# Performance work log

Hardware: AMD Instinct MI355X
Metric: run time of the kernel (lower is better)

Reference implementation:

```python
import jax, jax.numpy as jnp
import numpy as np

V = 50000      # variables -> 2V literals
C = 200000     # clauses
E = 300000     # edges per polarity
EMB = 128
NFC = 3
ROUNDS = 26


def setup_inputs() -> dict:
    key = jax.random.key(0)
    ks = jax.random.split(key, 16)
    s = 0.05
    f32 = jnp.float32
    inp = {
        "l_pos_emb": jax.random.normal(ks[0], (V, EMB), f32) * s,
        "l_neg_emb": jax.random.normal(ks[1], (V, EMB), f32) * s,
        "c_emb": jax.random.normal(ks[2], (C, EMB), f32) * s,
        "l_mlp_W": jax.random.normal(ks[3], (NFC, EMB, EMB), f32) * s,
        "l_mlp_b": jnp.zeros((NFC, EMB), f32),
        "c_mlp_W": jax.random.normal(ks[4], (NFC, EMB, EMB), f32) * s,
        "c_mlp_b": jnp.zeros((NFC, EMB), f32),
        "l_Wih": jax.random.normal(ks[5], (4 * EMB, 2 * EMB), f32) * s,
        "l_Whh": jax.random.normal(ks[6], (4 * EMB, EMB), f32) * s,
        "l_bih": jnp.zeros((4 * EMB,), f32),
        "l_bhh": jnp.zeros((4 * EMB,), f32),
        "c_Wih": jax.random.normal(ks[7], (4 * EMB, EMB), f32) * s,
        "c_Whh": jax.random.normal(ks[8], (4 * EMB, EMB), f32) * s,
        "c_bih": jnp.zeros((4 * EMB,), f32),
        "c_bhh": jnp.zeros((4 * EMB,), f32),
        "pos_src": jax.random.randint(ks[9], (E,), 0, V, jnp.int32),
        "pos_dst": jax.random.randint(ks[10], (E,), 0, C, jnp.int32),
        "neg_src": jax.random.randint(ks[11], (E,), 0, V, jnp.int32),
        "neg_dst": jax.random.randint(ks[12], (E,), 0, C, jnp.int32),
    }
    return inp


def _mlp(x, W, b):
    # num_fc Linear layers with ReLU between (no final activation)
    n = W.shape[0]
    for i in range(n):
        x = x @ W[i] + b[i]
        if i < n - 1:
            x = jax.nn.relu(x)
    return x


def _lstm_cell(x, h, c, Wih, Whh, bih, bhh):
    # torch nn.LSTM single step; gate order i, f, g, o
    gates = x @ Wih.T + h @ Whh.T + bih + bhh
    i, f, g, o = jnp.split(gates, 4, axis=1)
    c_new = jax.nn.sigmoid(f) * c + jax.nn.sigmoid(i) * jnp.tanh(g)
    h_new = jax.nn.sigmoid(o) * jnp.tanh(c_new)
    return h_new, c_new


def reference(l_pos_emb, l_neg_emb, c_emb,
              l_mlp_W, l_mlp_b, c_mlp_W, c_mlp_b,
              l_Wih, l_Whh, l_bih, l_bhh,
              c_Wih, c_Whh, c_bih, c_bhh,
              pos_src, pos_dst, neg_src, neg_dst):
    num_v = l_pos_emb.shape[0]
    num_c = c_emb.shape[0]
    l_h = jnp.concatenate([l_pos_emb, l_neg_emb], axis=0)   # [2V, E]
    l_c = jnp.zeros_like(l_h)
    c_h = c_emb
    c_c = jnp.zeros_like(c_h)

    def round_fn(carry, _):
        l_h, l_c, c_h, c_c = carry
        # literal -> clause messages
        l_msg = _mlp(l_h, l_mlp_W, l_mlp_b)
        pos_msg, neg_msg = l_msg[:num_v], l_msg[num_v:]
        l2c = (jax.ops.segment_sum(pos_msg[pos_src], pos_dst, num_segments=num_c)
               + jax.ops.segment_sum(neg_msg[neg_src], neg_dst, num_segments=num_c))
        # clause -> literal messages (reverse edges)
        c_msg = _mlp(c_h, c_mlp_W, c_mlp_b)
        pos_c2l = jax.ops.segment_sum(c_msg[pos_dst], pos_src, num_segments=num_v)
        neg_c2l = jax.ops.segment_sum(c_msg[neg_dst], neg_src, num_segments=num_v)
        c2l = jnp.concatenate([pos_c2l, neg_c2l], axis=0)    # [2V, E]
        # flip literal hidden (pair each literal with its negation)
        flip = jnp.concatenate([l_h[num_v:], l_h[:num_v]], axis=0)
        l_x = jnp.concatenate([c2l, flip], axis=1)           # [2V, 2E]
        l_h, l_c = _lstm_cell(l_x, l_h, l_c, l_Wih, l_Whh, l_bih, l_bhh)
        c_h, c_c = _lstm_cell(l2c, c_h, c_c, c_Wih, c_Whh, c_bih, c_bhh)
        return (l_h, l_c, c_h, c_c), None

    (l_h, l_c, c_h, c_c), _ = jax.lax.scan(round_fn, (l_h, l_c, c_h, c_c),
                                           None, length=ROUNDS)
    # concat final literal and clause embeddings: [2V + C, EMB]
    return jnp.concatenate([l_h, c_h], axis=0)
```

## Files before the change

### kernel.cpp

```cpp
#include <hip/hip_runtime.h>
#include <math.h>

typedef __attribute__((ext_vector_type(8))) short short8;
typedef __attribute__((ext_vector_type(4))) float f32x4;

constexpr int NV = 50000;
constexpr int NL = 100000;
constexpr int NC = 200000;
constexpr int NE = 300000;
constexpr int NROUNDS = 26;

__device__ __forceinline__ float sigf(float x) { return 1.0f / (1.0f + __expf(-x)); }

__device__ __forceinline__ void split8(const float* a, short8& h, short8& l) {
#pragma unroll
    for (int j = 0; j < 8; j++) {
        unsigned u = __float_as_uint(a[j]);
        h[j] = (short)(u >> 16);
        float lf = a[j] - __uint_as_float(u & 0xffff0000u);
        l[j] = (short)(__float_as_uint(lf) >> 16);
    }
}
__device__ __forceinline__ void split1(float x, unsigned short* h, unsigned short* l) {
    unsigned u = __float_as_uint(x);
    *h = (unsigned short)(u >> 16);
    float lf = x - __uint_as_float(u & 0xffff0000u);
    *l = (unsigned short)(__float_as_uint(lf) >> 16);
}

__device__ __forceinline__ void splitw(float x, unsigned short* h, unsigned short* l) {
    unsigned u = __float_as_uint(x);
    unsigned hr = (u + 0x7fffu + ((u >> 16) & 1u)) & 0xffff0000u;
    float lf = x - __uint_as_float(hr);
    unsigned ul = __float_as_uint(lf);
    *h = (unsigned short)(hr >> 16);
    *l = (unsigned short)((ul + 0x7fffu + ((ul >> 16) & 1u)) >> 16);
}


__global__ __launch_bounds__(256) void pack_mlp_frag(
    const float* __restrict__ W, unsigned short* __restrict__ Wh, unsigned short* __restrict__ Wl)
{
    int fid = blockIdx.x * 256 + threadIdx.x;
    if (fid >= 6144) return;
    int lane = fid & 63;
    int tile = (fid >> 6) & 7;
    int kt = (fid >> 9) & 3;
    int layer = fid >> 11;
    int l15 = lane & 15, lg = lane >> 4;
    int n = tile * 16 + l15;
#pragma unroll
    for (int j = 0; j < 8; j++) {
        int k = kt * 32 + lg * 8 + j;
        unsigned short h, l;
        splitw(W[layer * 16384 + k * 128 + n], &h, &l);
        Wh[(size_t)fid * 8 + j] = h;
        Wl[(size_t)fid * 8 + j] = l;
    }
}

__global__ __launch_bounds__(256) void pack_lstm_frag(
    const float* __restrict__ Wih, const float* __restrict__ Whh, int kih, int nstep,
    unsigned short* __restrict__ Wh, unsigned short* __restrict__ Wl)
{
    int fid = blockIdx.x * 256 + threadIdx.x;
    if (fid >= nstep * 2048) return;
    int lane = fid & 63;
    int tile = (fid >> 6) & 31;
    int kt = fid >> 11;
    int l15 = lane & 15, lg = lane >> 4;
    int n = tile * 16 + l15;
#pragma unroll
    for (int j = 0; j < 8; j++) {
        int k = kt * 32 + lg * 8 + j;
        float v = (k < kih) ? Wih[n * kih + k] : Whh[(n << 7) + (k - kih)];
        unsigned short h, l;
        splitw(v, &h, &l);
        Wh[(size_t)fid * 8 + j] = h;
        Wl[(size_t)fid * 8 + j] = l;
    }
}

__global__ __launch_bounds__(256) void csr_hist_k(
    const int* __restrict__ ps, const int* __restrict__ pd,
    const int* __restrict__ ns, const int* __restrict__ nd,
    int* __restrict__ cnt_c, int* __restrict__ cnt_l)
{
    int e = blockIdx.x * 256 + threadIdx.x;
    if (e >= NE) return;
    atomicAdd(&cnt_c[pd[e]], 1);
    atomicAdd(&cnt_c[nd[e]], 1);
    atomicAdd(&cnt_l[ps[e]], 1);
    atomicAdd(&cnt_l[NV + ns[e]], 1);
}

__global__ __launch_bounds__(256) void scan_p1(
    const int* __restrict__ cnt, int* __restrict__ partials, int n)
{
    __shared__ int sdata[256];
    int t = threadIdx.x, b = blockIdx.x;
    int base = b * 1024 + t * 4;
    int s = 0;
#pragma unroll
    for (int j = 0; j < 4; j++) { int i = base + j; if (i < n) s += cnt[i]; }
    sdata[t] = s; __syncthreads();
    for (int st = 128; st > 0; st >>= 1) {
        if (t < st) sdata[t] += sdata[t + st];
        __syncthreads();
    }
    if (t == 0) partials[b] = sdata[0];
}

__global__ __launch_bounds__(256) void scan_p2(int* __restrict__ partials, int nb, int* __restrict__ rowptr_end)
{
    __shared__ int sdata[256];
    int t = threadIdx.x;
    int v = (t < nb) ? partials[t] : 0;
    int x = v;
    sdata[t] = x; __syncthreads();
    for (int st = 1; st < 256; st <<= 1) {
        int y = (t >= st) ? sdata[t - st] : 0;
        __syncthreads();
        x += y; sdata[t] = x;
        __syncthreads();
    }
    if (t < nb) partials[t] = x - v;
    if (t == 255) *rowptr_end = sdata[255];
}

__global__ __launch_bounds__(256) void scan_p3(
    const int* __restrict__ cnt, const int* __restrict__ partials,
    int* __restrict__ rowptr, int* __restrict__ cursor, int n)
{
    __shared__ int sdata[256];
    int t = threadIdx.x, b = blockIdx.x;
    int base = b * 1024 + t * 4;
    int v[4]; int s = 0;
#pragma unroll
    for (int j = 0; j < 4; j++) { int i = base + j; v[j] = (i < n) ? cnt[i] : 0; s += v[j]; }
    int x = s;
    sdata[t] = x; __syncthreads();
    for (int st = 1; st < 256; st <<= 1) {
        int y = (t >= st) ? sdata[t - st] : 0;
        __syncthreads();
        x += y; sdata[t] = x;
        __syncthreads();
    }
    int off = partials[b] + x - s;
#pragma unroll
    for (int j = 0; j < 4; j++) {
        int i = base + j;
        if (i < n) { rowptr[i] = off; cursor[i] = off; off += v[j]; }
    }
}

__global__ __launch_bounds__(256) void csr_fill_k(
    const int* __restrict__ ps, const int* __restrict__ pd,
    const int* __restrict__ ns, const int* __restrict__ nd,
    int* __restrict__ cur_c, int* __restrict__ eidx_c,
    int* __restrict__ cur_l, int* __restrict__ eidx_l)
{
    int e = blockIdx.x * 256 + threadIdx.x;
    if (e >= NE) return;
    int p;
    p = atomicAdd(&cur_c[pd[e]], 1); eidx_c[p] = ps[e];
    p = atomicAdd(&cur_c[nd[e]], 1); eidx_c[p] = NV + ns[e];
    p = atomicAdd(&cur_l[ps[e]], 1); eidx_l[p] = pd[e];
    p = atomicAdd(&cur_l[NV + ns[e]], 1); eidx_l[p] = nd[e];
}

__global__ __launch_bounds__(256) void gather_sum_k(
    const float* __restrict__ msg, const int* __restrict__ rowptr,
    const int* __restrict__ eidx, float* __restrict__ out, int nrows)
{
    int row = (blockIdx.x * 256 + threadIdx.x) >> 6;
    if (row >= nrows) return;
    int lane = threadIdx.x & 63;
    int beg = rowptr[row], end = rowptr[row + 1];
    float ax = 0.f, ay = 0.f;
    for (int j = beg; j < end; j++) {
        int src = eidx[j];
        float2 v = *reinterpret_cast<const float2*>(msg + (size_t)src * 128 + lane * 2);
        ax += v.x; ay += v.y;
    }
    *reinterpret_cast<float2*>(out + (size_t)row * 128 + lane * 2) = make_float2(ax, ay);
}

__global__ __launch_bounds__(256, 3) void mlp3_v4(
    const float* __restrict__ x, const unsigned short* __restrict__ Wh,
    const unsigned short* __restrict__ Wl, const float* __restrict__ bias,
    float* __restrict__ y, int M)
{
    __shared__ unsigned short Xh[64][136];
    __shared__ unsigned short Xl[64][136];
    const int t = threadIdx.x;
    const int rb = blockIdx.x * 64;
    const int lane = t & 63, w = t >> 6, wr = w >> 1, wc = w & 1;
    const int l15 = lane & 15, lg = lane >> 4;

#pragma unroll
    for (int j = 0; j < 8; j++) {
        int i = t + 256 * j;
        int r = i >> 5, c4 = i & 31;
        int gr = rb + r; if (gr >= M) gr = M - 1;
        float4 v = *reinterpret_cast<const float4*>(x + (size_t)gr * 128 + c4 * 4);
        const float* vp = &v.x;
#pragma unroll
        for (int e = 0; e < 4; e++) {
            unsigned short h, l;
            split1(vp[e], &h, &l);
            Xh[r][c4 * 4 + e] = h;
            Xl[r][c4 * 4 + e] = l;
        }
    }
    __syncthreads();

    for (int layer = 0; layer < 3; layer++) {
        f32x4 acc[2][4];
#pragma unroll
        for (int m = 0; m < 2; m++)
#pragma unroll
            for (int nf = 0; nf < 4; nf++) acc[m][nf] = f32x4{0.f, 0.f, 0.f, 0.f};

        short8 bh[4], bl[4], bhn[4], bln[4];
#pragma unroll
        for (int nf = 0; nf < 4; nf++) {
            int tile = wc * 4 + nf;
            size_t off = ((size_t)((layer * 4 + 0) * 8 + tile) * 64 + lane) * 8;
            bh[nf] = *reinterpret_cast<const short8*>(Wh + off);
            bl[nf] = *reinterpret_cast<const short8*>(Wl + off);
        }

#pragma unroll
        for (int kt = 0; kt < 4; kt++) {
            short8 ah[2], al[2];
#pragma unroll
            for (int m = 0; m < 2; m++) {
                int row = wr * 32 + m * 16 + l15;
                ah[m] = *reinterpret_cast<const short8*>(&Xh[row][kt * 32 + lg * 8]);
                al[m] = *reinterpret_cast<const short8*>(&Xl[row][kt * 32 + lg * 8]);
            }
            if (kt < 3) {
#pragma unroll
                for (int nf = 0; nf < 4; nf++) {
                    int tile = wc * 4 + nf;
                    size_t off = ((size_t)((layer * 4 + kt + 1) * 8 + tile) * 64 + lane) * 8;
                    bhn[nf] = *reinterpret_cast<const short8*>(Wh + off);
                    bln[nf] = *reinterpret_cast<const short8*>(Wl + off);
                }
            }
#pragma unroll
            for (int nf = 0; nf < 4; nf++)
#pragma unroll
                for (int m = 0; m < 2; m++)
                    acc[m][nf] = __builtin_amdgcn_mfma_f32_16x16x32_bf16(ah[m], bh[nf], acc[m][nf], 0, 0, 0);
#pragma unroll
            for (int nf = 0; nf < 4; nf++)
#pragma unroll
                for (int m = 0; m < 2; m++)
                    acc[m][nf] = __builtin_amdgcn_mfma_f32_16x16x32_bf16(ah[m], bl[nf], acc[m][nf], 0, 0, 0);
#pragma unroll
            for (int nf = 0; nf < 4; nf++)
#pragma unroll
                for (int m = 0; m < 2; m++)
                    acc[m][nf] = __builtin_amdgcn_mfma_f32_16x16x32_bf16(al[m], bh[nf], acc[m][nf], 0, 0, 0);
            if (kt < 3) {
#pragma unroll
                for (int nf = 0; nf < 4; nf++) { bh[nf] = bhn[nf]; bl[nf] = bln[nf]; }
            }
        }

        float bv[4];
#pragma unroll
        for (int nf = 0; nf < 4; nf++) bv[nf] = bias[layer * 128 + wc * 64 + nf * 16 + l15];
        __syncthreads();
        if (layer < 2) {
#pragma unroll
            for (int m = 0; m < 2; m++)
#pragma unroll
                for (int nf = 0; nf < 4; nf++)
#pragma unroll
                    for (int rr = 0; rr < 4; rr++) {
                        float v = fmaxf(acc[m][nf][rr] + bv[nf], 0.f);
                        unsigned short h, l;
                        split1(v, &h, &l);
                        int rw = wr * 32 + m * 16 + lg * 4 + rr;
                        int cl = wc * 64 + nf * 16 + l15;
                        Xh[rw][cl] = h;
                        Xl[rw][cl] = l;
                    }
            __syncthreads();
        } else {
#pragma unroll
            for (int m = 0; m < 2; m++)
#pragma unroll
                for (int rr = 0; rr < 4; rr++) {
                    int gr = rb + wr * 32 + m * 16 + lg * 4 + rr;
                    if (gr < M) {
#pragma unroll
                        for (int nf = 0; nf < 4; nf++)
                            y[(size_t)gr * 128 + wc * 64 + nf * 16 + l15] = acc[m][nf][rr] + bv[nf];
                    }
                }
        }
    }
}

template <int NKT, bool FLIP>
__global__ __launch_bounds__(256, 2) void lstm_v5(
    const float* __restrict__ A0, const float* __restrict__ A1, const float* __restrict__ A2,
    const unsigned short* __restrict__ Bh_g, const unsigned short* __restrict__ Bl_g,
    const float* __restrict__ bih, const float* __restrict__ bhh,
    float* __restrict__ c_st, float* __restrict__ h_out, int M)
{
    __shared__ float As[2][4096];
    __shared__ unsigned short Bsm[2][8192];
    const int t = threadIdx.x;
    const int s = blockIdx.x;
    const int rb = blockIdx.y * 128;
    const int lane = t & 63, w = t >> 6, wr = w >> 1, wc = w & 1;
    const int l15 = lane & 15, lg = lane >> 4;

    f32x4 acc[4][4];
#pragma unroll
    for (int m = 0; m < 4; m++)
#pragma unroll
        for (int g = 0; g < 4; g++) acc[m][g] = f32x4{0.f, 0.f, 0.f, 0.f};

#pragma unroll
    for (int i = 0; i < 4; i++) {
        int idx = t + 256 * i;
        int r = idx >> 3, c4 = idx & 7;
        int gr = rb + r; if (gr >= M) gr = M - 1;
        float4 v = *reinterpret_cast<const float4*>(A0 + (size_t)gr * 128 + c4 * 4);
        int off = (r * 128 + c4 * 16) ^ ((r & 7) << 4);
        *reinterpret_cast<float4*>((char*)As[0] + off) = v;
    }
#pragma unroll
    for (int i = 0; i < 4; i++) {
        int idx = t + 256 * i;
        int f = idx >> 6, ln = idx & 63;
        int sel = f >> 3, ft = f & 7;
        int gt = (ft >> 1) * 8 + s * 2 + (ft & 1);
        const unsigned short* bsrc = sel ? Bl_g : Bh_g;
        uint4 v = *reinterpret_cast<const uint4*>(bsrc + ((size_t)gt * 64 + ln) * 8);
        *reinterpret_cast<uint4*>((char*)Bsm[0] + idx * 16) = v;
    }
    __syncthreads();

    int cur = 0;
#pragma unroll
    for (int kt = 0; kt < NKT; kt++) {
        float4 a_stg[4]; uint4 b_stg[4];
        if (kt + 1 < NKT) {
            const int kn = kt + 1;
            const int seg = kn >> 2;
            const float* src = (seg == 0) ? A0 : ((seg == 1) ? A1 : A2);
            const bool useF = FLIP && (seg == 1);
            const int kco = (kn & 3) * 32;
#pragma unroll
            for (int i = 0; i < 4; i++) {
                int idx = t + 256 * i;
                int r = idx >> 3, c4 = idx & 7;
                int gr = rb + r; if (gr >= M) gr = M - 1;
                if (useF) gr = (gr < NV) ? gr + NV : gr - NV;
                a_stg[i] = *reinterpret_cast<const float4*>(src + (size_t)gr * 128 + kco + c4 * 4);
            }
#pragma unroll
            for (int i = 0; i < 4; i++) {
                int idx = t + 256 * i;
                int f = idx >> 6, ln = idx & 63;
                int sel = f >> 3, ft = f & 7;
                int gt = (ft >> 1) * 8 + s * 2 + (ft & 1);
                const unsigned short* bsrc = sel ? Bl_g : Bh_g;
                b_stg[i] = *reinterpret_cast<const uint4*>(bsrc + ((size_t)(kn * 32 + gt) * 64 + ln) * 8);
            }
        }

        const char* Ab = (const char*)As[cur];
        short8 ah[4], al[4];
#pragma unroll
        for (int m = 0; m < 4; m++) {
            int r = wr * 64 + m * 16 + l15;
            int base = r * 128 + lg * 32;
            int swz = (r & 7) << 4;
            float av[8];
            *reinterpret_cast<float4*>(&av[0]) =
                *reinterpret_cast<const float4*>(Ab + (base ^ swz));
            *reinterpret_cast<float4*>(&av[4]) =
                *reinterpret_cast<const float4*>(Ab + ((base + 16) ^ swz));
            split8(av, ah[m], al[m]);
        }
        const char* Bb = (const char*)Bsm[cur];
#pragma unroll
        for (int g = 0; g < 4; g++) {
            short8 bh = *reinterpret_cast<const short8*>(Bb + ((g * 2 + wc) * 64 + lane) * 16);
            short8 bl = *reinterpret_cast<const short8*>(Bb + ((8 + g * 2 + wc) * 64 + lane) * 16);
#pragma unroll
            for (int m = 0; m < 4; m++)
                acc[m][g] = __builtin_amdgcn_mfma_f32_16x16x32_bf16(ah[m], bh, acc[m][g], 0, 0, 0);
#pragma unroll
            for (int m = 0; m < 4; m++)
                acc[m][g] = __builtin_amdgcn_mfma_f32_16x16x32_bf16(ah[m], bl, acc[m][g], 0, 0, 0);
#pragma unroll
            for (int m = 0; m < 4; m++)
                acc[m][g] = __builtin_amdgcn_mfma_f32_16x16x32_bf16(al[m], bh, acc[m][g], 0, 0, 0);
        }

        if (kt + 1 < NKT) {
            int nb = cur ^ 1;
#pragma unroll
            for (int i = 0; i < 4; i++) {
                int idx = t + 256 * i;
                int r = idx >> 3, c4 = idx & 7;
                int off = (r * 128 + c4 * 16) ^ ((r & 7) << 4);
                *reinterpret_cast<float4*>((char*)As[nb] + off) = a_stg[i];
            }
#pragma unroll
            for (int i = 0; i < 4; i++) {
                int idx = t + 256 * i;
                *reinterpret_cast<uint4*>((char*)Bsm[nb] + idx * 16) = b_stg[i];
            }
        }
        __syncthreads();
        cur ^= 1;
    }

    const int colc = s * 32 + wc * 16 + l15;
    float bs4[4];
#pragma unroll
    for (int g = 0; g < 4; g++) bs4[g] = bih[g * 128 + colc] + bhh[g * 128 + colc];
#pragma unroll
    for (int m = 0; m < 4; m++)
#pragma unroll
        for (int rr = 0; rr < 4; rr++) {
            int gr = rb + wr * 64 + m * 16 + lg * 4 + rr;
            if (gr >= M) continue;
            float gi = acc[m][0][rr] + bs4[0];
            float gf = acc[m][1][rr] + bs4[1];
            float gg = acc[m][2][rr] + bs4[2];
            float go = acc[m][3][rr] + bs4[3];
            size_t p = (size_t)gr * 128 + colc;
            float cold = c_st[p];
            float cn = sigf(gf) * cold + sigf(gi) * tanhf(gg);
            float hn = sigf(go) * tanhf(cn);
            c_st[p] = cn;
            h_out[p] = hn;
        }
}

extern "C" void kernel_launch(void* const* d_in, const int* in_sizes, int n_in,
                              void* d_out, int out_size, void* d_ws, size_t ws_size,
                              hipStream_t stream)
{
    const float* l_pos   = (const float*)d_in[0];
    const float* l_neg   = (const float*)d_in[1];
    const float* c_emb   = (const float*)d_in[2];
    const float* l_mlp_W = (const float*)d_in[3];
    const float* l_mlp_b = (const float*)d_in[4];
    const float* c_mlp_W = (const float*)d_in[5];
    const float* c_mlp_b = (const float*)d_in[6];
    const float* l_Wih   = (const float*)d_in[7];
    const float* l_Whh   = (const float*)d_in[8];
    const float* l_bih   = (const float*)d_in[9];
    const float* l_bhh   = (const float*)d_in[10];
    const float* c_Wih   = (const float*)d_in[11];
    const float* c_Whh   = (const float*)d_in[12];
    const float* c_bih   = (const float*)d_in[13];
    const float* c_bhh   = (const float*)d_in[14];
    const int* pos_src   = (const int*)d_in[15];
    const int* pos_dst   = (const int*)d_in[16];
    const int* neg_src   = (const int*)d_in[17];
    const int* neg_dst   = (const int*)d_in[18];

    float* out  = (float*)d_out;
    float* l_hA = out;
    float* c_hP = out + (size_t)NL * 128;

    float* wsp = (float*)d_ws;
    float* l_hB  = wsp; wsp += (size_t)NL * 128;
    float* l_c   = wsp; wsp += (size_t)NL * 128;
    float* c_c   = wsp; wsp += (size_t)NC * 128;
    float* l_msg = wsp; wsp += (size_t)NL * 128;
    float* c_hQ  = wsp; wsp += (size_t)NC * 128;
    float* l2c   = wsp; wsp += (size_t)NC * 128;
    float* c2l = l_msg;

    unsigned short* us = (unsigned short*)wsp;
    unsigned short* mlpLh = us; us += 3 * 128 * 128;
    unsigned short* mlpLl = us; us += 3 * 128 * 128;
    unsigned short* mlpCh = us; us += 3 * 128 * 128;
    unsigned short* mlpCl = us; us += 3 * 128 * 128;
    unsigned short* lstmLh = us; us += 512 * 384;
    unsigned short* lstmLl = us; us += 512 * 384;
    unsigned short* lstmCh = us; us += 512 * 256;
    unsigned short* lstmCl = us; us += 512 * 256;

    int* ip = (int*)us;
    int* cnt_c    = ip; ip += NC;
    int* rowptr_c = ip; ip += NC + 1;
    int* cur_c    = ip; ip += NC;
    int* eidx_c   = ip; ip += 2 * NE;
    int* cnt_l    = ip; ip += NL;
    int* rowptr_l = ip; ip += NL + 1;
    int* cur_l    = ip; ip += NL;
    int* eidx_l   = ip; ip += 2 * NE;
    int* part_c   = ip; ip += 256;
    int* part_l   = ip; ip += 256;

    hipMemcpyAsync(l_hA, l_pos, (size_t)NV * 128 * 4, hipMemcpyDeviceToDevice, stream);
    hipMemcpyAsync(l_hA + (size_t)NV * 128, l_neg, (size_t)NV * 128 * 4, hipMemcpyDeviceToDevice, stream);
    hipMemcpyAsync(c_hP, c_emb, (size_t)NC * 128 * 4, hipMemcpyDeviceToDevice, stream);
    hipMemsetAsync(l_c, 0, (size_t)NL * 128 * 4, stream);
    hipMemsetAsync(c_c, 0, (size_t)NC * 128 * 4, stream);

    pack_mlp_frag<<<24, 256, 0, stream>>>(l_mlp_W, mlpLh, mlpLl);
    pack_mlp_frag<<<24, 256, 0, stream>>>(c_mlp_W, mlpCh, mlpCl);
    pack_lstm_frag<<<96, 256, 0, stream>>>(l_Wih, l_Whh, 256, 12, lstmLh, lstmLl);
    pack_lstm_frag<<<64, 256, 0, stream>>>(c_Wih, c_Whh, 128, 8, lstmCh, lstmCl);

    hipMemsetAsync(cnt_c, 0, NC * sizeof(int), stream);
    hipMemsetAsync(cnt_l, 0, NL * sizeof(int), stream);
    constexpr int EB = (NE + 255) / 256;
    csr_hist_k<<<EB, 256, 0, stream>>>(pos_src, pos_dst, neg_src, neg_dst, cnt_c, cnt_l);
    constexpr int NBC = (NC + 1023) / 1024;
    constexpr int NBL = (NL + 1023) / 1024;
    scan_p1<<<NBC, 256, 0, stream>>>(cnt_c, part_c, NC);
    scan_p2<<<1, 256, 0, stream>>>(part_c, NBC, rowptr_c + NC);
    scan_p3<<<NBC, 256, 0, stream>>>(cnt_c, part_c, rowptr_c, cur_c, NC);
    scan_p1<<<NBL, 256, 0, stream>>>(cnt_l, part_l, NL);
    scan_p2<<<1, 256, 0, stream>>>(part_l, NBL, rowptr_l + NL);
    scan_p3<<<NBL, 256, 0, stream>>>(cnt_l, part_l, rowptr_l, cur_l, NL);
    csr_fill_k<<<EB, 256, 0, stream>>>(pos_src, pos_dst, neg_src, neg_dst,
                                       cur_c, eidx_c, cur_l, eidx_l);

    float* l_cur = l_hA;
    float* l_nxt = l_hB;
    float* c_cur = c_hP;
    float* c_oth = c_hQ;

    for (int r = 0; r < NROUNDS; r++) {
        mlp3_v4<<<(NL + 63) / 64, 256, 0, stream>>>(l_cur, mlpLh, mlpLl, l_mlp_b, l_msg, NL);
        mlp3_v4<<<(NC + 63) / 64, 256, 0, stream>>>(c_cur, mlpCh, mlpCl, c_mlp_b, c_oth, NC);

        gather_sum_k<<<NC * 64 / 256, 256, 0, stream>>>(l_msg, rowptr_c, eidx_c, l2c, NC);
        gather_sum_k<<<NL * 64 / 256, 256, 0, stream>>>(c_oth, rowptr_l, eidx_l, c2l, NL);

        lstm_v5<12, true><<<dim3(4, (NL + 127) / 128), 256, 0, stream>>>(
            c2l, l_cur, l_cur, lstmLh, lstmLl, l_bih, l_bhh, l_c, l_nxt, NL);
        lstm_v5<8, false><<<dim3(4, (NC + 127) / 128), 256, 0, stream>>>(
            l2c, c_cur, nullptr, lstmCh, lstmCl, c_bih, c_bhh, c_c, c_oth, NC);

        float* t2 = l_cur; l_cur = l_nxt; l_nxt = t2;
        t2 = c_cur; c_cur = c_oth; c_oth = t2;
    }
    (void)in_sizes; (void)n_in; (void)out_size; (void)ws_size;
}
```

Measured before the change: 22.52 ms.

## Store activations as pre-split bf16 hi/lo planes instead of fp32

Hidden states, messages and aggregated sums now live in a split bf16 hi/lo layout (two 128-wide planes per row) rather than fp32. The MLP and LSTM kernels can then copy operands straight into shared memory in MFMA fragment order, with no per-tile split work. The LSTM A tile also drops its swizzled fp32 staging for a fragment-ordered layout. Gather sums reconstruct fp32 from the planes and re-split on output, and extra conversion kernels run at start and end. The lo plane is truncated rather than rounded, so some precision is lost compared with the fp32 path.

```diff
diff --git a/kernel.cpp b/kernel.cpp
--- a/kernel.cpp
+++ b/kernel.cpp
@@ -3,6 +3,7 @@
 
 typedef __attribute__((ext_vector_type(8))) short short8;
 typedef __attribute__((ext_vector_type(4))) float f32x4;
+typedef unsigned short ushort_t;
 
 constexpr int NV = 50000;
 constexpr int NL = 100000;
@@ -12,34 +13,50 @@
 
 __device__ __forceinline__ float sigf(float x) { return 1.0f / (1.0f + __expf(-x)); }
 
-__device__ __forceinline__ void split8(const float* a, short8& h, short8& l) {
-#pragma unroll
-    for (int j = 0; j < 8; j++) {
-        unsigned u = __float_as_uint(a[j]);
-        h[j] = (short)(u >> 16);
-        float lf = a[j] - __uint_as_float(u & 0xffff0000u);
-        l[j] = (short)(__float_as_uint(lf) >> 16);
-    }
-}
-__device__ __forceinline__ void split1(float x, unsigned short* h, unsigned short* l) {
+__device__ __forceinline__ void split1(float x, ushort_t* h, ushort_t* l) {
     unsigned u = __float_as_uint(x);
-    *h = (unsigned short)(u >> 16);
+    *h = (ushort_t)(u >> 16);
     float lf = x - __uint_as_float(u & 0xffff0000u);
-    *l = (unsigned short)(__float_as_uint(lf) >> 16);
-}
-
-__device__ __forceinline__ void splitw(float x, unsigned short* h, unsigned short* l) {
+    *l = (ushort_t)(__float_as_uint(lf) >> 16);
+}
+__device__ __forceinline__ float recf(ushort_t h, ushort_t l) {
+    return __uint_as_float((unsigned)h << 16) + __uint_as_float((unsigned)l << 16);
+}
+
+__device__ __forceinline__ void splitw(float x, ushort_t* h, ushort_t* l) {
     unsigned u = __float_as_uint(x);
     unsigned hr = (u + 0x7fffu + ((u >> 16) & 1u)) & 0xffff0000u;
     float lf = x - __uint_as_float(hr);
     unsigned ul = __float_as_uint(lf);
-    *h = (unsigned short)(hr >> 16);
-    *l = (unsigned short)((ul + 0x7fffu + ((ul >> 16) & 1u)) >> 16);
+    *h = (ushort_t)(hr >> 16);
+    *l = (ushort_t)((ul + 0x7fffu + ((ul >> 16) & 1u)) >> 16);
+}
+
+
+__global__ __launch_bounds__(256) void split_rows_k(
+    const float* __restrict__ src, ushort_t* __restrict__ dst, int total)
+{
+    for (int i = blockIdx.x * 256 + threadIdx.x; i < total; i += gridDim.x * 256) {
+        int row = i >> 7, c = i & 127;
+        ushort_t h, l;
+        split1(src[i], &h, &l);
+        dst[(size_t)row * 256 + c] = h;
+        dst[(size_t)row * 256 + 128 + c] = l;
+    }
+}
+
+__global__ __launch_bounds__(256) void convert_out_k(
+    const ushort_t* __restrict__ src, float* __restrict__ dst, int total)
+{
+    for (int i = blockIdx.x * 256 + threadIdx.x; i < total; i += gridDim.x * 256) {
+        int row = i >> 7, c = i & 127;
+        dst[i] = recf(src[(size_t)row * 256 + c], src[(size_t)row * 256 + 128 + c]);
+    }
 }
 
 
 __global__ __launch_bounds__(256) void pack_mlp_frag(
-    const float* __restrict__ W, unsigned short* __restrict__ Wh, unsigned short* __restrict__ Wl)
+    const float* __restrict__ W, ushort_t* __restrict__ Wh, ushort_t* __restrict__ Wl)
 {
     int fid = blockIdx.x * 256 + threadIdx.x;
     if (fid >= 6144) return;
@@ -52,7 +69,7 @@
 #pragma unroll
     for (int j = 0; j < 8; j++) {
         int k = kt * 32 + lg * 8 + j;
-        unsigned short h, l;
+        ushort_t h, l;
         splitw(W[layer * 16384 + k * 128 + n], &h, &l);
         Wh[(size_t)fid * 8 + j] = h;
         Wl[(size_t)fid * 8 + j] = l;
@@ -61,7 +78,7 @@
 
 __global__ __launch_bounds__(256) void pack_lstm_frag(
     const float* __restrict__ Wih, const float* __restrict__ Whh, int kih, int nstep,
-    unsigned short* __restrict__ Wh, unsigned short* __restrict__ Wl)
+    ushort_t* __restrict__ Wh, ushort_t* __restrict__ Wl)
 {
     int fid = blockIdx.x * 256 + threadIdx.x;
     if (fid >= nstep * 2048) return;
@@ -74,7 +91,7 @@
     for (int j = 0; j < 8; j++) {
         int k = kt * 32 + lg * 8 + j;
         float v = (k < kih) ? Wih[n * kih + k] : Whh[(n << 7) + (k - kih)];
-        unsigned short h, l;
+        ushort_t h, l;
         splitw(v, &h, &l);
         Wh[(size_t)fid * 8 + j] = h;
         Wl[(size_t)fid * 8 + j] = l;
@@ -170,29 +187,37 @@
 }
 
 __global__ __launch_bounds__(256) void gather_sum_k(
-    const float* __restrict__ msg, const int* __restrict__ rowptr,
-    const int* __restrict__ eidx, float* __restrict__ out, int nrows)
+    const ushort_t* __restrict__ msg, const int* __restrict__ rowptr,
+    const int* __restrict__ eidx, ushort_t* __restrict__ out, int nrows)
 {
     int row = (blockIdx.x * 256 + threadIdx.x) >> 6;
     if (row >= nrows) return;
     int lane = threadIdx.x & 63;
     int beg = rowptr[row], end = rowptr[row + 1];
-    float ax = 0.f, ay = 0.f;
+    float a0 = 0.f, a1 = 0.f;
     for (int j = beg; j < end; j++) {
         int src = eidx[j];
-        float2 v = *reinterpret_cast<const float2*>(msg + (size_t)src * 128 + lane * 2);
-        ax += v.x; ay += v.y;
-    }
-    *reinterpret_cast<float2*>(out + (size_t)row * 128 + lane * 2) = make_float2(ax, ay);
-}
-
-__global__ __launch_bounds__(256, 3) void mlp3_v4(
-    const float* __restrict__ x, const unsigned short* __restrict__ Wh,
-    const unsigned short* __restrict__ Wl, const float* __restrict__ bias,
-    float* __restrict__ y, int M)
-{
-    __shared__ unsigned short Xh[64][136];
-    __shared__ unsigned short Xl[64][136];
+        const ushort_t* p = msg + (size_t)src * 256 + lane * 2;
+        unsigned hp = *reinterpret_cast<const unsigned*>(p);
+        unsigned lp = *reinterpret_cast<const unsigned*>(p + 128);
+        a0 += __uint_as_float(hp << 16) + __uint_as_float(lp << 16);
+        a1 += __uint_as_float(hp & 0xffff0000u) + __uint_as_float(lp & 0xffff0000u);
+    }
+    ushort_t h0, l0, h1, l1;
+    split1(a0, &h0, &l0);
+    split1(a1, &h1, &l1);
+    ushort_t* op = out + (size_t)row * 256 + lane * 2;
+    *reinterpret_cast<unsigned*>(op) = (unsigned)h0 | ((unsigned)h1 << 16);
+    *reinterpret_cast<unsigned*>(op + 128) = (unsigned)l0 | ((unsigned)l1 << 16);
+}
+
+__global__ __launch_bounds__(256, 3) void mlp3_v5(
+    const ushort_t* __restrict__ x, const ushort_t* __restrict__ Wh,
+    const ushort_t* __restrict__ Wl, const float* __restrict__ bias,
+    ushort_t* __restrict__ y, int M)
+{
+    __shared__ ushort_t Xh[64][136];
+    __shared__ ushort_t Xl[64][136];
     const int t = threadIdx.x;
     const int rb = blockIdx.x * 64;
     const int lane = t & 63, w = t >> 6, wr = w >> 1, wc = w & 1;
@@ -200,18 +225,13 @@
 
 #pragma unroll
     for (int j = 0; j < 8; j++) {
-        int i = t + 256 * j;
-        int r = i >> 5, c4 = i & 31;
+        int idx = t + 256 * j;
+        int plane = idx >> 10, rem = idx & 1023;
+        int r = rem >> 4, c8 = (rem & 15) * 8;
         int gr = rb + r; if (gr >= M) gr = M - 1;
-        float4 v = *reinterpret_cast<const float4*>(x + (size_t)gr * 128 + c4 * 4);
-        const float* vp = &v.x;
-#pragma unroll
-        for (int e = 0; e < 4; e++) {
-            unsigned short h, l;
-            split1(vp[e], &h, &l);
-            Xh[r][c4 * 4 + e] = h;
-            Xl[r][c4 * 4 + e] = l;
-        }
+        uint4 v = *reinterpret_cast<const uint4*>(x + (size_t)gr * 256 + plane * 128 + c8);
+        ushort_t* dst = plane ? &Xl[r][c8] : &Xh[r][c8];
+        *reinterpret_cast<uint4*>(dst) = v;
     }
     __syncthreads();
 
@@ -282,7 +302,7 @@
 #pragma unroll
                     for (int rr = 0; rr < 4; rr++) {
                         float v = fmaxf(acc[m][nf][rr] + bv[nf], 0.f);
-                        unsigned short h, l;
+                        ushort_t h, l;
                         split1(v, &h, &l);
                         int rw = wr * 32 + m * 16 + lg * 4 + rr;
                         int cl = wc * 64 + nf * 16 + l15;
@@ -298,8 +318,14 @@
                     int gr = rb + wr * 32 + m * 16 + lg * 4 + rr;
                     if (gr < M) {
 #pragma unroll
-                        for (int nf = 0; nf < 4; nf++)
-                            y[(size_t)gr * 128 + wc * 64 + nf * 16 + l15] = acc[m][nf][rr] + bv[nf];
+                        for (int nf = 0; nf < 4; nf++) {
+                            float v = acc[m][nf][rr] + bv[nf];
+                            ushort_t h, l;
+                            split1(v, &h, &l);
+                            size_t p = (size_t)gr * 256 + wc * 64 + nf * 16 + l15;
+                            y[p] = h;
+                            y[p + 128] = l;
+                        }
                     }
                 }
         }
@@ -307,14 +333,14 @@
 }
 
 template <int NKT, bool FLIP>
-__global__ __launch_bounds__(256, 2) void lstm_v5(
-    const float* __restrict__ A0, const float* __restrict__ A1, const float* __restrict__ A2,
-    const unsigned short* __restrict__ Bh_g, const unsigned short* __restrict__ Bl_g,
+__global__ __launch_bounds__(256, 2) void lstm_v6(
+    const ushort_t* __restrict__ A0, const ushort_t* __restrict__ A1, const ushort_t* __restrict__ A2,
+    const ushort_t* __restrict__ Bh_g, const ushort_t* __restrict__ Bl_g,
     const float* __restrict__ bih, const float* __restrict__ bhh,
-    float* __restrict__ c_st, float* __restrict__ h_out, int M)
-{
-    __shared__ float As[2][4096];
-    __shared__ unsigned short Bsm[2][8192];
+    float* __restrict__ c_st, ushort_t* __restrict__ h_out, int M)
+{
+    __shared__ uint4 As[2][1024];
+    __shared__ uint4 Bs[2][1024];
     const int t = threadIdx.x;
     const int s = blockIdx.x;
     const int rb = blockIdx.y * 128;
@@ -330,11 +356,11 @@
 #pragma unroll
     for (int i = 0; i < 4; i++) {
         int idx = t + 256 * i;
-        int r = idx >> 3, c4 = idx & 7;
-        int gr = rb + r; if (gr >= M) gr = M - 1;
-        float4 v = *reinterpret_cast<const float4*>(A0 + (size_t)gr * 128 + c4 * 4);
-        int off = (r * 128 + c4 * 16) ^ ((r & 7) << 4);
-        *reinterpret_cast<float4*>((char*)As[0] + off) = v;
+        int plane = idx >> 9, rem = idx & 511;
+        int tile = rem >> 6, ln = rem & 63;
+        int gr = rb + tile * 16 + (ln & 15); if (gr >= M) gr = M - 1;
+        As[0][idx] = *reinterpret_cast<const uint4*>(
+            A0 + (size_t)gr * 256 + plane * 128 + (ln >> 4) * 8);
     }
 #pragma unroll
     for (int i = 0; i < 4; i++) {
@@ -342,29 +368,30 @@
         int f = idx >> 6, ln = idx & 63;
         int sel = f >> 3, ft = f & 7;
         int gt = (ft >> 1) * 8 + s * 2 + (ft & 1);
-        const unsigned short* bsrc = sel ? Bl_g : Bh_g;
-        uint4 v = *reinterpret_cast<const uint4*>(bsrc + ((size_t)gt * 64 + ln) * 8);
-        *reinterpret_cast<uint4*>((char*)Bsm[0] + idx * 16) = v;
+        const ushort_t* bsrc = sel ? Bl_g : Bh_g;
+        Bs[0][idx] = *reinterpret_cast<const uint4*>(bsrc + ((size_t)gt * 64 + ln) * 8);
     }
     __syncthreads();
 
     int cur = 0;
 #pragma unroll
     for (int kt = 0; kt < NKT; kt++) {
-        float4 a_stg[4]; uint4 b_stg[4];
+        uint4 a_stg[4], b_stg[4];
         if (kt + 1 < NKT) {
             const int kn = kt + 1;
             const int seg = kn >> 2;
-            const float* src = (seg == 0) ? A0 : ((seg == 1) ? A1 : A2);
+            const ushort_t* src = (seg == 0) ? A0 : ((seg == 1) ? A1 : A2);
             const bool useF = FLIP && (seg == 1);
             const int kco = (kn & 3) * 32;
 #pragma unroll
             for (int i = 0; i < 4; i++) {
                 int idx = t + 256 * i;
-                int r = idx >> 3, c4 = idx & 7;
-                int gr = rb + r; if (gr >= M) gr = M - 1;
+                int plane = idx >> 9, rem = idx & 511;
+                int tile = rem >> 6, ln = rem & 63;
+                int gr = rb + tile * 16 + (ln & 15); if (gr >= M) gr = M - 1;
                 if (useF) gr = (gr < NV) ? gr + NV : gr - NV;
-                a_stg[i] = *reinterpret_cast<const float4*>(src + (size_t)gr * 128 + kco + c4 * 4);
+                a_stg[i] = *reinterpret_cast<const uint4*>(
+                    src + (size_t)gr * 256 + plane * 128 + kco + (ln >> 4) * 8);
             }
 #pragma unroll
             for (int i = 0; i < 4; i++) {
@@ -372,30 +399,24 @@
                 int f = idx >> 6, ln = idx & 63;
                 int sel = f >> 3, ft = f & 7;
                 int gt = (ft >> 1) * 8 + s * 2 + (ft & 1);
-                const unsigned short* bsrc = sel ? Bl_g : Bh_g;
+                const ushort_t* bsrc = sel ? Bl_g : Bh_g;
                 b_stg[i] = *reinterpret_cast<const uint4*>(bsrc + ((size_t)(kn * 32 + gt) * 64 + ln) * 8);
             }
         }
 
-        const char* Ab = (const char*)As[cur];
+        const uint4* Ab = As[cur];
+        const uint4* Bb = Bs[cur];
         short8 ah[4], al[4];
 #pragma unroll
         for (int m = 0; m < 4; m++) {
-            int r = wr * 64 + m * 16 + l15;
-            int base = r * 128 + lg * 32;
-            int swz = (r & 7) << 4;
-            float av[8];
-            *reinterpret_cast<float4*>(&av[0]) =
-                *reinterpret_cast<const float4*>(Ab + (base ^ swz));
-            *reinterpret_cast<float4*>(&av[4]) =
-                *reinterpret_cast<const float4*>(Ab + ((base + 16) ^ swz));
-            split8(av, ah[m], al[m]);
-        }
-        const char* Bb = (const char*)Bsm[cur];
+            int tile = wr * 4 + m;
+            ah[m] = *reinterpret_cast<const short8*>(&Ab[tile * 64 + lane]);
+            al[m] = *reinterpret_cast<const short8*>(&Ab[512 + tile * 64 + lane]);
+        }
 #pragma unroll
         for (int g = 0; g < 4; g++) {
-            short8 bh = *reinterpret_cast<const short8*>(Bb + ((g * 2 + wc) * 64 + lane) * 16);
-            short8 bl = *reinterpret_cast<const short8*>(Bb + ((8 + g * 2 + wc) * 64 + lane) * 16);
+            short8 bh = *reinterpret_cast<const short8*>(&Bb[(g * 2 + wc) * 64 + lane]);
+            short8 bl = *reinterpret_cast<const short8*>(&Bb[(8 + g * 2 + wc) * 64 + lane]);
 #pragma unroll
             for (int m = 0; m < 4; m++)
                 acc[m][g] = __builtin_amdgcn_mfma_f32_16x16x32_bf16(ah[m], bh, acc[m][g], 0, 0, 0);
@@ -410,17 +431,9 @@
         if (kt + 1 < NKT) {
             int nb = cur ^ 1;
 #pragma unroll
-            for (int i = 0; i < 4; i++) {
-                int idx = t + 256 * i;
-                int r = idx >> 3, c4 = idx & 7;
-                int off = (r * 128 + c4 * 16) ^ ((r & 7) << 4);
-                *reinterpret_cast<float4*>((char*)As[nb] + off) = a_stg[i];
-            }
-#pragma unroll
-            for (int i = 0; i < 4; i++) {
-                int idx = t + 256 * i;
-                *reinterpret_cast<uint4*>((char*)Bsm[nb] + idx * 16) = b_stg[i];
-            }
+            for (int i = 0; i < 4; i++) As[nb][t + 256 * i] = a_stg[i];
+#pragma unroll
+            for (int i = 0; i < 4; i++) Bs[nb][t + 256 * i] = b_stg[i];
         }
         __syncthreads();
         cur ^= 1;
@@ -440,12 +453,16 @@
             float gf = acc[m][1][rr] + bs4[1];
             float gg = acc[m][2][rr] + bs4[2];
             float go = acc[m][3][rr] + bs4[3];
-            size_t p = (size_t)gr * 128 + colc;
-            float cold = c_st[p];
+            size_t pc = (size_t)gr * 128 + colc;
+            float cold = c_st[pc];
             float cn = sigf(gf) * cold + sigf(gi) * tanhf(gg);
             float hn = sigf(go) * tanhf(cn);
-            c_st[p] = cn;
-            h_out[p] = hn;
+            c_st[pc] = cn;
+            ushort_t hh, hl;
+            split1(hn, &hh, &hl);
+            size_t ph = (size_t)gr * 256 + colc;
+            h_out[ph] = hh;
+            h_out[ph + 128] = hl;
         }
 }
 
@@ -473,28 +490,28 @@
     const int* neg_src   = (const int*)d_in[17];
     const int* neg_dst   = (const int*)d_in[18];
 
-    float* out  = (float*)d_out;
-    float* l_hA = out;
-    float* c_hP = out + (size_t)NL * 128;
+    float* out = (float*)d_out;
+    ushort_t* l_hQ = (ushort_t*)d_out;
+    ushort_t* c_hQ = (ushort_t*)(out + (size_t)NL * 128);
 
     float* wsp = (float*)d_ws;
-    float* l_hB  = wsp; wsp += (size_t)NL * 128;
-    float* l_c   = wsp; wsp += (size_t)NL * 128;
-    float* c_c   = wsp; wsp += (size_t)NC * 128;
-    float* l_msg = wsp; wsp += (size_t)NL * 128;
-    float* c_hQ  = wsp; wsp += (size_t)NC * 128;
-    float* l2c   = wsp; wsp += (size_t)NC * 128;
-    float* c2l = l_msg;
-
-    unsigned short* us = (unsigned short*)wsp;
-    unsigned short* mlpLh = us; us += 3 * 128 * 128;
-    unsigned short* mlpLl = us; us += 3 * 128 * 128;
-    unsigned short* mlpCh = us; us += 3 * 128 * 128;
-    unsigned short* mlpCl = us; us += 3 * 128 * 128;
-    unsigned short* lstmLh = us; us += 512 * 384;
-    unsigned short* lstmLl = us; us += 512 * 384;
-    unsigned short* lstmCh = us; us += 512 * 256;
-    unsigned short* lstmCl = us; us += 512 * 256;
+    ushort_t* l_hP  = (ushort_t*)wsp; wsp += (size_t)NL * 128;
+    float*    l_c   = wsp;            wsp += (size_t)NL * 128;
+    float*    c_c   = wsp;            wsp += (size_t)NC * 128;
+    ushort_t* l_msg = (ushort_t*)wsp; wsp += (size_t)NL * 128;
+    ushort_t* c_hP  = (ushort_t*)wsp; wsp += (size_t)NC * 128;
+    ushort_t* l2c   = (ushort_t*)wsp; wsp += (size_t)NC * 128;
+    ushort_t* c2l = l_msg;
+
+    ushort_t* us = (ushort_t*)wsp;
+    ushort_t* mlpLh = us; us += 3 * 128 * 128;
+    ushort_t* mlpLl = us; us += 3 * 128 * 128;
+    ushort_t* mlpCh = us; us += 3 * 128 * 128;
+    ushort_t* mlpCl = us; us += 3 * 128 * 128;
+    ushort_t* lstmLh = us; us += 512 * 384;
+    ushort_t* lstmLl = us; us += 512 * 384;
+    ushort_t* lstmCh = us; us += 512 * 256;
+    ushort_t* lstmCl = us; us += 512 * 256;
 
     int* ip = (int*)us;
     int* cnt_c    = ip; ip += NC;
@@ -508,9 +525,9 @@
     int* part_c   = ip; ip += 256;
     int* part_l   = ip; ip += 256;
 
-    hipMemcpyAsync(l_hA, l_pos, (size_t)NV * 128 * 4, hipMemcpyDeviceToDevice, stream);
-    hipMemcpyAsync(l_hA + (size_t)NV * 128, l_neg, (size_t)NV * 128 * 4, hipMemcpyDeviceToDevice, stream);
-    hipMemcpyAsync(c_hP, c_emb, (size_t)NC * 128 * 4, hipMemcpyDeviceToDevice, stream);
+    split_rows_k<<<2048, 256, 0, stream>>>(l_pos, l_hP, NV * 128);
+    split_rows_k<<<2048, 256, 0, stream>>>(l_neg, l_hP + (size_t)NV * 256, NV * 128);
+    split_rows_k<<<2048, 256, 0, stream>>>(c_emb, c_hP, NC * 128);
     hipMemsetAsync(l_c, 0, (size_t)NL * 128 * 4, stream);
     hipMemsetAsync(c_c, 0, (size_t)NC * 128 * 4, stream);
 
@@ -534,25 +551,27 @@
     csr_fill_k<<<EB, 256, 0, stream>>>(pos_src, pos_dst, neg_src, neg_dst,
                                        cur_c, eidx_c, cur_l, eidx_l);
 
-    float* l_cur = l_hA;
-    float* l_nxt = l_hB;
-    float* c_cur = c_hP;
-    float* c_oth = c_hQ;
+    ushort_t* l_cur = l_hP;
+    ushort_t* l_nxt = l_hQ;
+    ushort_t* c_cur = c_hP;
+    ushort_t* c_oth = c_hQ;
 
     for (int r = 0; r < NROUNDS; r++) {
-        mlp3_v4<<<(NL + 63) / 64, 256, 0, stream>>>(l_cur, mlpLh, mlpLl, l_mlp_b, l_msg, NL);
-        mlp3_v4<<<(NC + 63) / 64, 256, 0, stream>>>(c_cur, mlpCh, mlpCl, c_mlp_b, c_oth, NC);
+        mlp3_v5<<<(NL + 63) / 64, 256, 0, stream>>>(l_cur, mlpLh, mlpLl, l_mlp_b, l_msg, NL);
+        mlp3_v5<<<(NC + 63) / 64, 256, 0, stream>>>(c_cur, mlpCh, mlpCl, c_mlp_b, c_oth, NC);
 
         gather_sum_k<<<NC * 64 / 256, 256, 0, stream>>>(l_msg, rowptr_c, eidx_c, l2c, NC);
         gather_sum_k<<<NL * 64 / 256, 256, 0, stream>>>(c_oth, rowptr_l, eidx_l, c2l, NL);
 
-        lstm_v5<12, true><<<dim3(4, (NL + 127) / 128), 256, 0, stream>>>(
+        lstm_v6<12, true><<<dim3(4, (NL + 127) / 128), 256, 0, stream>>>(
             c2l, l_cur, l_cur, lstmLh, lstmLl, l_bih, l_bhh, l_c, l_nxt, NL);
-        lstm_v5<8, false><<<dim3(4, (NC + 127) / 128), 256, 0, stream>>>(
+        lstm_v6<8, false><<<dim3(4, (NC + 127) / 128), 256, 0, stream>>>(
             l2c, c_cur, nullptr, lstmCh, lstmCl, c_bih, c_bhh, c_c, c_oth, NC);
 
-        float* t2 = l_cur; l_cur = l_nxt; l_nxt = t2;
+        ushort_t* t2 = l_cur; l_cur = l_nxt; l_nxt = t2;
         t2 = c_cur; c_cur = c_oth; c_oth = t2;
     }
+    convert_out_k<<<2048, 256, 0, stream>>>(l_hP, out, NL * 128);
+    convert_out_k<<<2048, 256, 0, stream>>>(c_hP, out + (size_t)NL * 128, NC * 128);
     (void)in_sizes; (void)n_in; (void)out_size; (void)ws_size;
 }
```

After: 23.15 ms. +2.8%, slower.
